# Kernel tuning notes

Hardware: AMD Instinct MI355X
Metric: run time of the kernel (lower is better)

## Reference

```python
import jax, jax.numpy as jnp
import numpy as np

N_NODES = 100000
N_EDGES = 600000
D_IN = 128
D_HID = 128
D_OUT = 64


def setup_inputs() -> dict:
    key = jax.random.key(0)
    ks = jax.random.split(key, 6)
    x = jax.random.normal(ks[0], (N_NODES, D_IN), dtype=jnp.float32)
    edge_index = jax.random.randint(ks[1], (2, N_EDGES), 0, N_NODES, dtype=jnp.int32)
    # Glorot-ish init for GCNConv weights
    W1 = jax.random.normal(ks[2], (D_IN, D_HID), dtype=jnp.float32) * (1.0 / np.sqrt(D_IN))
    W2 = jax.random.normal(ks[3], (D_HID, D_HID), dtype=jnp.float32) * (1.0 / np.sqrt(D_HID))
    W3 = jax.random.normal(ks[4], (D_HID, D_OUT), dtype=jnp.float32) * (1.0 / np.sqrt(D_HID))
    b1 = jnp.zeros((D_HID,), dtype=jnp.float32)
    b2 = jnp.zeros((D_HID,), dtype=jnp.float32)
    b3 = jnp.zeros((D_OUT,), dtype=jnp.float32)
    return {"x": x, "edge_index": edge_index, "W1": W1, "b1": b1,
            "W2": W2, "b2": b2, "W3": W3, "b3": b3}


def reference(x, edge_index, W1, b1, W2, b2, W3, b3):
    N = x.shape[0]
    # PyG GCNConv default: add self-loops, symmetric degree normalization.
    row, col = edge_index[0], edge_index[1]
    loops = jnp.arange(N, dtype=row.dtype)
    row = jnp.concatenate([row, loops])  # source nodes
    col = jnp.concatenate([col, loops])  # destination nodes (aggregation target)
    deg = jax.ops.segment_sum(jnp.ones(row.shape, dtype=x.dtype), col, num_segments=N)
    dinv = jax.lax.rsqrt(jnp.maximum(deg, 1.0))  # deg >= 1 due to self-loops
    norm = dinv[row] * dinv[col]  # [E+N]

    def gcn_conv(h, W, b):
        hw = h @ W                                   # dense transform [N, D]
        msg = hw[row] * norm[:, None]                # gather + normalize [E+N, D]
        return jax.ops.segment_sum(msg, col, num_segments=N) + b  # scatter-add

    h = jax.nn.relu(gcn_conv(x, W1, b1))
    # dropout p=0.5 is identity in eval mode (training=False)
    h = jax.nn.relu(gcn_conv(h, W2, b2))
    h = gcn_conv(h, W3, b3)
    return jax.nn.log_softmax(h, axis=1)
```

## Files before the change

### kernel.cpp

```cpp
#include <hip/hip_runtime.h>

#define NN 100000
#define NE 600000

typedef unsigned short u16;
typedef float f32x4 __attribute__((ext_vector_type(4)));
typedef short s16x8 __attribute__((ext_vector_type(8)));

__device__ inline u16 f2bf(float f) {
    unsigned u = __float_as_uint(f);
    return (u16)((u + 0x7FFFu + ((u >> 16) & 1u)) >> 16);
}
__device__ inline float bflo(unsigned u) { return __uint_as_float(u << 16); }
__device__ inline float bfhi(unsigned u) { return __uint_as_float(u & 0xFFFF0000u); }
__device__ inline unsigned pk(float a, float b) {
    return (unsigned)f2bf(a) | ((unsigned)f2bf(b) << 16);
}


__global__ void k_init_deg(int* __restrict__ deg, int n) {
    int i = blockIdx.x * 256 + threadIdx.x;
    if (i < n) deg[i] = 0;
}

__global__ void k_deg_count(const int* __restrict__ col, int* __restrict__ deg, int E) {
    int e = blockIdx.x * 256 + threadIdx.x;
    if (e < E) atomicAdd(&deg[col[e]], 1);
}

__global__ void k_scan1(const int* __restrict__ deg, int* __restrict__ offs,
                        int* __restrict__ bsums, float* __restrict__ dinv, int n) {
    __shared__ int s[256];
    int t = threadIdx.x;
    int i = blockIdx.x * 256 + t;
    int v = (i < n) ? deg[i] : 0;
    if (i < n) dinv[i] = rsqrtf((float)(v + 1));
    s[t] = v;
    __syncthreads();
    for (int off = 1; off < 256; off <<= 1) {
        int x = (t >= off) ? s[t - off] : 0;
        __syncthreads();
        s[t] += x;
        __syncthreads();
    }
    if (i < n) offs[i] = s[t] - v;
    if (t == 255) bsums[blockIdx.x] = s[255];
}

__global__ void k_scan2(int* __restrict__ bsums, int nb) {
    __shared__ int s[512];
    int t = threadIdx.x;
    int v = (t < nb) ? bsums[t] : 0;
    s[t] = v;
    __syncthreads();
    for (int off = 1; off < 512; off <<= 1) {
        int x = (t >= off) ? s[t - off] : 0;
        __syncthreads();
        s[t] += x;
        __syncthreads();
    }
    if (t < nb) bsums[t] = s[t] - v;
}

__global__ void k_scan3(int* __restrict__ offs, const int* __restrict__ bsums,
                        int* __restrict__ cursor, int n) {
    int i = blockIdx.x * 256 + threadIdx.x;
    if (i < n) {
        int o = offs[i] + bsums[i >> 8];
        offs[i] = o;
        cursor[i] = o;
    }
}

__global__ void k_fill(const int* __restrict__ row, const int* __restrict__ col,
                       int* __restrict__ cursor, int* __restrict__ srcs, int E) {
    int e = blockIdx.x * 256 + threadIdx.x;
    if (e < E) {
        int p = atomicAdd(&cursor[col[e]], 1);
        srcs[p] = row[e];
    }
}


__device__ inline void pack_one(const float* W, u16* Wp, int g, int DOUT) {
    int i  = g & 7;
    int l  = (g >> 3) & 63;
    int kk = (g >> 9) & 3;
    int t  = g >> 11;
    int k = kk * 32 + ((l >> 4) << 3) + i;
    int c = t * 16 + (l & 15);
    Wp[g] = f2bf(W[k * DOUT + c]);
}

__global__ __launch_bounds__(256)
void k_pack_all(const float* __restrict__ W1, const float* __restrict__ W2,
                const float* __restrict__ W3, u16* __restrict__ wp1,
                u16* __restrict__ wp2, u16* __restrict__ wp3) {
    int gid = blockIdx.x * 256 + threadIdx.x;
    if (gid < 16384) pack_one(W1, wp1, gid, 128);
    else if (gid < 32768) pack_one(W2, wp2, gid - 16384, 128);
    else if (gid < 40960) pack_one(W3, wp3, gid - 32768, 64);
}


template <int DOUT, bool OB16, bool AF32>
__global__ __launch_bounds__(256)
void k_gemm_mfma(const void* __restrict__ Hin, const u16* __restrict__ Wp,
                 const float* __restrict__ dinv, void* __restrict__ Gout, int n) {
    constexpr int NT = DOUT / 16;
    int tid = threadIdx.x;
    int w = tid >> 6, l = tid & 63;
    int r0 = blockIdx.x * 128 + w * 32;
    int arow0 = r0 + (l & 15);
    int arow1 = arow0 + 16;
    bool av0 = arow0 < n, av1 = arow1 < n;
    const s16x8* A0 = (const s16x8*)((const u16*)Hin + (size_t)arow0 * 128);
    const s16x8* A1 = (const s16x8*)((const u16*)Hin + (size_t)arow1 * 128);
    const float* A032 = (const float*)Hin + (size_t)arow0 * 128;
    const float* A132 = (const float*)Hin + (size_t)arow1 * 128;
    const s16x8* Wp8 = (const s16x8*)Wp;
    const s16x8 zero = {0, 0, 0, 0, 0, 0, 0, 0};

    f32x4 acc0[NT], acc1[NT];
#pragma unroll
    for (int t = 0; t < NT; t++) { acc0[t] = {0.f,0.f,0.f,0.f}; acc1[t] = {0.f,0.f,0.f,0.f}; }

#pragma unroll
    for (int kk = 0; kk < 4; kk++) {
        s16x8 a0, a1;
        if (AF32) {
            a0 = zero; a1 = zero;
            if (av0) {
                const f32x4* p = (const f32x4*)(A032 + kk * 32 + ((l >> 4) << 3));
                f32x4 f0 = p[0], f1 = p[1];
                a0[0]=(short)f2bf(f0[0]); a0[1]=(short)f2bf(f0[1]);
                a0[2]=(short)f2bf(f0[2]); a0[3]=(short)f2bf(f0[3]);
                a0[4]=(short)f2bf(f1[0]); a0[5]=(short)f2bf(f1[1]);
                a0[6]=(short)f2bf(f1[2]); a0[7]=(short)f2bf(f1[3]);
            }
            if (av1) {
                const f32x4* p = (const f32x4*)(A132 + kk * 32 + ((l >> 4) << 3));
                f32x4 f0 = p[0], f1 = p[1];
                a1[0]=(short)f2bf(f0[0]); a1[1]=(short)f2bf(f0[1]);
                a1[2]=(short)f2bf(f0[2]); a1[3]=(short)f2bf(f0[3]);
                a1[4]=(short)f2bf(f1[0]); a1[5]=(short)f2bf(f1[1]);
                a1[6]=(short)f2bf(f1[2]); a1[7]=(short)f2bf(f1[3]);
            }
        } else {
            a0 = av0 ? A0[kk * 4 + (l >> 4)] : zero;
            a1 = av1 ? A1[kk * 4 + (l >> 4)] : zero;
        }
#pragma unroll
        for (int t = 0; t < NT; t++) {
            s16x8 b = Wp8[(t * 4 + kk) * 64 + l];
            acc0[t] = __builtin_amdgcn_mfma_f32_16x16x32_bf16(a0, b, acc0[t], 0, 0, 0);
            acc1[t] = __builtin_amdgcn_mfma_f32_16x16x32_bf16(a1, b, acc1[t], 0, 0, 0);
        }
    }

    int col = l & 15;
#pragma unroll
    for (int r = 0; r < 4; r++) {
        int gr0 = r0 + (l >> 4) * 4 + r;
        if (gr0 < n) {
            float di = dinv[gr0];
#pragma unroll
            for (int t = 0; t < NT; t++) {
                float v = acc0[t][r] * di;
                if (OB16) ((u16*)Gout)[(size_t)gr0 * DOUT + t * 16 + col] = f2bf(v);
                else      ((float*)Gout)[(size_t)gr0 * DOUT + t * 16 + col] = v;
            }
        }
        int gr1 = gr0 + 16;
        if (gr1 < n) {
            float di = dinv[gr1];
#pragma unroll
            for (int t = 0; t < NT; t++) {
                float v = acc1[t][r] * di;
                if (OB16) ((u16*)Gout)[(size_t)gr1 * DOUT + t * 16 + col] = f2bf(v);
                else      ((float*)Gout)[(size_t)gr1 * DOUT + t * 16 + col] = v;
            }
        }
    }
}


#define ACC8(A, U) \
    A[0] += bflo(U.x); A[1] += bfhi(U.x); A[2] += bflo(U.y); A[3] += bfhi(U.y); \
    A[4] += bflo(U.z); A[5] += bfhi(U.z); A[6] += bflo(U.w); A[7] += bfhi(U.w);

__global__ __launch_bounds__(256)
void k_agg_relu(const uint4* __restrict__ G, const int* __restrict__ offs,
                const int* __restrict__ deg, const int* __restrict__ srcs,
                const float* __restrict__ dinv, const float* __restrict__ bias,
                uint4* __restrict__ out, int n) {
    int t = blockIdx.x * 256 + threadIdx.x;
    int wv = t >> 6;
    int lane = t & 63;
    int hl = lane & 15;
    int node = wv * 4 + (lane >> 4);
    if (node >= n) return;

    uint4 us = G[(size_t)node * 16 + hl];
    float a0[8], a1[8], a2[8], a3[8];
    a0[0] = bflo(us.x); a0[1] = bfhi(us.x); a0[2] = bflo(us.y); a0[3] = bfhi(us.y);
    a0[4] = bflo(us.z); a0[5] = bfhi(us.z); a0[6] = bflo(us.w); a0[7] = bfhi(us.w);
#pragma unroll
    for (int i = 0; i < 8; i++) { a1[i] = 0.f; a2[i] = 0.f; a3[i] = 0.f; }

    int start = offs[node];
    int cnt = deg[node];
    int j = 0;
    for (; j + 4 <= cnt; j += 4) {
        int s0 = srcs[start + j + 0];
        int s1 = srcs[start + j + 1];
        int s2 = srcs[start + j + 2];
        int s3 = srcs[start + j + 3];
        uint4 u0 = G[(size_t)s0 * 16 + hl];
        uint4 u1 = G[(size_t)s1 * 16 + hl];
        uint4 u2 = G[(size_t)s2 * 16 + hl];
        uint4 u3 = G[(size_t)s3 * 16 + hl];
        ACC8(a0, u0) ACC8(a1, u1) ACC8(a2, u2) ACC8(a3, u3)
    }
    for (; j < cnt; j++) {
        int s = srcs[start + j];
        uint4 u = G[(size_t)s * 16 + hl];
        ACC8(a0, u)
    }

    float di = dinv[node];
    const float4* b8 = (const float4*)bias;
    float4 b0 = b8[hl * 2], b1 = b8[hl * 2 + 1];
    float bb[8] = {b0.x, b0.y, b0.z, b0.w, b1.x, b1.y, b1.z, b1.w};
    float r[8];
#pragma unroll
    for (int i = 0; i < 8; i++) {
        float s = (a0[i] + a1[i]) + (a2[i] + a3[i]);
        r[i] = fmaxf(fmaf(s, di, bb[i]), 0.f);
    }
    out[(size_t)node * 16 + hl] =
        make_uint4(pk(r[0], r[1]), pk(r[2], r[3]), pk(r[4], r[5]), pk(r[6], r[7]));
}

#define ACC4(A, U) \
    A[0] += bflo(U.x); A[1] += bfhi(U.x); A[2] += bflo(U.y); A[3] += bfhi(U.y);

__global__ __launch_bounds__(256)
void k_agg_softmax(const uint2* __restrict__ G, const int* __restrict__ offs,
                   const int* __restrict__ deg, const int* __restrict__ srcs,
                   const float* __restrict__ dinv, const float* __restrict__ bias,
                   float4* __restrict__ out, int n) {
    int t = blockIdx.x * 256 + threadIdx.x;
    int wv = t >> 6;
    int lane = t & 63;
    int hl = lane & 15;
    int node = wv * 4 + (lane >> 4);
    if (node >= n) return;

    uint2 us = G[(size_t)node * 16 + hl];
    float a0[4], a1[4], a2[4], a3[4];
    a0[0] = bflo(us.x); a0[1] = bfhi(us.x); a0[2] = bflo(us.y); a0[3] = bfhi(us.y);
#pragma unroll
    for (int i = 0; i < 4; i++) { a1[i] = 0.f; a2[i] = 0.f; a3[i] = 0.f; }

    int start = offs[node];
    int cnt = deg[node];
    int j = 0;
    for (; j + 4 <= cnt; j += 4) {
        int s0 = srcs[start + j + 0];
        int s1 = srcs[start + j + 1];
        int s2 = srcs[start + j + 2];
        int s3 = srcs[start + j + 3];
        uint2 u0 = G[(size_t)s0 * 16 + hl];
        uint2 u1 = G[(size_t)s1 * 16 + hl];
        uint2 u2 = G[(size_t)s2 * 16 + hl];
        uint2 u3 = G[(size_t)s3 * 16 + hl];
        ACC4(a0, u0) ACC4(a1, u1) ACC4(a2, u2) ACC4(a3, u3)
    }
    for (; j < cnt; j++) {
        int s = srcs[start + j];
        uint2 u = G[(size_t)s * 16 + hl];
        ACC4(a0, u)
    }

    float di = dinv[node];
    float4 bb = ((const float4*)bias)[hl];
    float t0 = fmaf((a0[0] + a1[0]) + (a2[0] + a3[0]), di, bb.x);
    float t1 = fmaf((a0[1] + a1[1]) + (a2[1] + a3[1]), di, bb.y);
    float t2 = fmaf((a0[2] + a1[2]) + (a2[2] + a3[2]), di, bb.z);
    float t3 = fmaf((a0[3] + a1[3]) + (a2[3] + a3[3]), di, bb.w);
    float m = fmaxf(fmaxf(t0, t1), fmaxf(t2, t3));
#pragma unroll
    for (int off = 1; off < 16; off <<= 1) m = fmaxf(m, __shfl_xor(m, off, 64));
    float e = expf(t0 - m) + expf(t1 - m) + expf(t2 - m) + expf(t3 - m);
#pragma unroll
    for (int off = 1; off < 16; off <<= 1) e += __shfl_xor(e, off, 64);
    float lse = m + logf(e);
    out[(size_t)node * 16 + hl] = make_float4(t0 - lse, t1 - lse, t2 - lse, t3 - lse);
}


extern "C" void kernel_launch(void* const* d_in, const int* in_sizes, int n_in,
                              void* d_out, int out_size, void* d_ws, size_t ws_size,
                              hipStream_t stream) {
    const float* x  = (const float*)d_in[0];
    const int*   ei = (const int*)d_in[1];
    const int*   row = ei;
    const int*   col = ei + NE;
    const float* W1 = (const float*)d_in[2];
    const float* b1 = (const float*)d_in[3];
    const float* W2 = (const float*)d_in[4];
    const float* b2 = (const float*)d_in[5];
    const float* W3 = (const float*)d_in[6];
    const float* b3 = (const float*)d_in[7];
    float* outp = (float*)d_out;

    char* ws = (char*)d_ws;
    size_t off = 0;
    auto alloc = [&](size_t bytes) -> void* {
        void* p = (void*)(ws + off);
        off += (bytes + 255) & ~(size_t)255;
        return p;
    };
    float* dinv  = (float*)alloc((size_t)NN * 4);
    float* bufA  = (float*)alloc((size_t)NN * 128 * 4);
    u16*   bufB  = (u16*)alloc((size_t)NN * 128 * 2);
    int*   deg   = (int*)alloc((size_t)NN * 4);
    int*   offs  = (int*)alloc((size_t)NN * 4);
    int*   cursor= (int*)alloc((size_t)NN * 4);
    int*   bsums = (int*)alloc(1024 * 4);
    int*   srcs  = (int*)alloc((size_t)NE * 4);
    u16*   wp1   = (u16*)alloc(128 * 128 * 2);
    u16*   wp2   = (u16*)alloc(128 * 128 * 2);
    u16*   wp3   = (u16*)alloc(128 * 64 * 2);

    int nbN = (NN + 255) / 256;
    int nbE = (NE + 255) / 256;

    k_init_deg <<<nbN, 256, 0, stream>>>(deg, NN);
    k_deg_count<<<nbE, 256, 0, stream>>>(col, deg, NE);
    k_scan1    <<<nbN, 256, 0, stream>>>(deg, offs, bsums, dinv, NN);
    k_scan2    <<<1,   512, 0, stream>>>(bsums, nbN);
    k_scan3    <<<nbN, 256, 0, stream>>>(offs, bsums, cursor, NN);
    k_fill     <<<nbE, 256, 0, stream>>>(row, col, cursor, srcs, NE);
    k_pack_all <<<160, 256, 0, stream>>>(W1, W2, W3, wp1, wp2, wp3);

    int gb = (NN + 127) / 128;
    int ab4 = ((NN + 3) / 4 * 64 + 255) / 256;

    k_gemm_mfma<128, true, true><<<gb, 256, 0, stream>>>(x, wp1, dinv, bufA, NN);
    k_agg_relu <<<ab4, 256, 0, stream>>>((uint4*)bufA, offs, deg, srcs, dinv, b1, (uint4*)bufB, NN);
    k_gemm_mfma<128, true, false><<<gb, 256, 0, stream>>>(bufB, wp2, dinv, bufA, NN);
    k_agg_relu <<<ab4, 256, 0, stream>>>((uint4*)bufA, offs, deg, srcs, dinv, b2, (uint4*)bufB, NN);
    k_gemm_mfma<64, true, false><<<gb, 256, 0, stream>>>(bufB, wp3, dinv, bufA, NN);
    k_agg_softmax<<<ab4, 256, 0, stream>>>((uint2*)bufA, offs, deg, srcs, dinv, b3, (float4*)outp, NN);
}
```

Baseline: 310.8 us.

## Pad CSR neighbor lists to multiples of eight with zero sentinel row

Each node's CSR segment is rounded up to a multiple of eight and padded with a sentinel index pointing to a zeroed extra row of the feature buffer. The aggregation kernels can then load indices as two int4 vectors and issue eight gathers per iteration with no remainder loop. The layer-3 feature buffer now uses a row stride of 128 so the sentinel row lines up. This adds a padding kernel, larger index storage and wasted gathers on padded slots, and replaces the degree init kernel with a memset.

Measured after the change: 304.8 us. Within noise of the previous version (-1.9%).

```diff
diff --git a/kernel.cpp b/kernel.cpp
--- a/kernel.cpp
+++ b/kernel.cpp
@@ -17,11 +17,6 @@
     return (unsigned)f2bf(a) | ((unsigned)f2bf(b) << 16);
 }
 
-
-__global__ void k_init_deg(int* __restrict__ deg, int n) {
-    int i = blockIdx.x * 256 + threadIdx.x;
-    if (i < n) deg[i] = 0;
-}
 
 __global__ void k_deg_count(const int* __restrict__ col, int* __restrict__ deg, int E) {
     int e = blockIdx.x * 256 + threadIdx.x;
@@ -33,8 +28,9 @@
     __shared__ int s[256];
     int t = threadIdx.x;
     int i = blockIdx.x * 256 + t;
-    int v = (i < n) ? deg[i] : 0;
-    if (i < n) dinv[i] = rsqrtf((float)(v + 1));
+    int d = (i < n) ? deg[i] : 0;
+    int v = (i < n) ? (((d + 7) >> 3) << 3) : 0;
+    if (i < n) dinv[i] = rsqrtf((float)(d + 1));
     s[t] = v;
     __syncthreads();
     for (int off = 1; off < 256; off <<= 1) {
@@ -81,6 +77,17 @@
     }
 }
 
+__global__ void k_pad(const int* __restrict__ deg, const int* __restrict__ offs,
+                      int* __restrict__ srcs, int n) {
+    int i = blockIdx.x * 256 + threadIdx.x;
+    if (i < n) {
+        int d = deg[i];
+        int pd = ((d + 7) >> 3) << 3;
+        int o = offs[i] + d;
+        for (int j = d; j < pd; j++) srcs[o++] = NN;
+    }
+}
+
 
 __device__ inline void pack_one(const float* W, u16* Wp, int g, int DOUT) {
     int i  = g & 7;
@@ -95,11 +102,13 @@
 __global__ __launch_bounds__(256)
 void k_pack_all(const float* __restrict__ W1, const float* __restrict__ W2,
                 const float* __restrict__ W3, u16* __restrict__ wp1,
-                u16* __restrict__ wp2, u16* __restrict__ wp3) {
+                u16* __restrict__ wp2, u16* __restrict__ wp3,
+                uint4* __restrict__ bufA) {
     int gid = blockIdx.x * 256 + threadIdx.x;
     if (gid < 16384) pack_one(W1, wp1, gid, 128);
     else if (gid < 32768) pack_one(W2, wp2, gid - 16384, 128);
     else if (gid < 40960) pack_one(W3, wp3, gid - 32768, 64);
+    else if (gid < 40976) bufA[(size_t)NN * 16 + (gid - 40960)] = make_uint4(0, 0, 0, 0);
 }
 
 
@@ -167,8 +176,8 @@
 #pragma unroll
             for (int t = 0; t < NT; t++) {
                 float v = acc0[t][r] * di;
-                if (OB16) ((u16*)Gout)[(size_t)gr0 * DOUT + t * 16 + col] = f2bf(v);
-                else      ((float*)Gout)[(size_t)gr0 * DOUT + t * 16 + col] = v;
+                if (OB16) ((u16*)Gout)[(size_t)gr0 * 128 + t * 16 + col] = f2bf(v);
+                else      ((float*)Gout)[(size_t)gr0 * 128 + t * 16 + col] = v;
             }
         }
         int gr1 = gr0 + 16;
@@ -177,8 +186,8 @@
 #pragma unroll
             for (int t = 0; t < NT; t++) {
                 float v = acc1[t][r] * di;
-                if (OB16) ((u16*)Gout)[(size_t)gr1 * DOUT + t * 16 + col] = f2bf(v);
-                else      ((float*)Gout)[(size_t)gr1 * DOUT + t * 16 + col] = v;
+                if (OB16) ((u16*)Gout)[(size_t)gr1 * 128 + t * 16 + col] = f2bf(v);
+                else      ((float*)Gout)[(size_t)gr1 * 128 + t * 16 + col] = v;
             }
         }
     }
@@ -209,23 +218,20 @@
     for (int i = 0; i < 8; i++) { a1[i] = 0.f; a2[i] = 0.f; a3[i] = 0.f; }
 
     int start = offs[node];
-    int cnt = deg[node];
-    int j = 0;
-    for (; j + 4 <= cnt; j += 4) {
-        int s0 = srcs[start + j + 0];
-        int s1 = srcs[start + j + 1];
-        int s2 = srcs[start + j + 2];
-        int s3 = srcs[start + j + 3];
-        uint4 u0 = G[(size_t)s0 * 16 + hl];
-        uint4 u1 = G[(size_t)s1 * 16 + hl];
-        uint4 u2 = G[(size_t)s2 * 16 + hl];
-        uint4 u3 = G[(size_t)s3 * 16 + hl];
+    int nb = (deg[node] + 7) >> 3;
+    for (int b = 0; b < nb; b++) {
+        const int4* ip = (const int4*)&srcs[start + b * 8];
+        int4 i0 = ip[0], i1 = ip[1];
+        uint4 u0 = G[(size_t)i0.x * 16 + hl];
+        uint4 u1 = G[(size_t)i0.y * 16 + hl];
+        uint4 u2 = G[(size_t)i0.z * 16 + hl];
+        uint4 u3 = G[(size_t)i0.w * 16 + hl];
+        uint4 u4 = G[(size_t)i1.x * 16 + hl];
+        uint4 u5 = G[(size_t)i1.y * 16 + hl];
+        uint4 u6 = G[(size_t)i1.z * 16 + hl];
+        uint4 u7 = G[(size_t)i1.w * 16 + hl];
         ACC8(a0, u0) ACC8(a1, u1) ACC8(a2, u2) ACC8(a3, u3)
-    }
-    for (; j < cnt; j++) {
-        int s = srcs[start + j];
-        uint4 u = G[(size_t)s * 16 + hl];
-        ACC8(a0, u)
+        ACC8(a0, u4) ACC8(a1, u5) ACC8(a2, u6) ACC8(a3, u7)
     }
 
     float di = dinv[node];
@@ -257,30 +263,27 @@
     int node = wv * 4 + (lane >> 4);
     if (node >= n) return;
 
-    uint2 us = G[(size_t)node * 16 + hl];
+    uint2 us = G[(size_t)node * 32 + hl];
     float a0[4], a1[4], a2[4], a3[4];
     a0[0] = bflo(us.x); a0[1] = bfhi(us.x); a0[2] = bflo(us.y); a0[3] = bfhi(us.y);
 #pragma unroll
     for (int i = 0; i < 4; i++) { a1[i] = 0.f; a2[i] = 0.f; a3[i] = 0.f; }
 
     int start = offs[node];
-    int cnt = deg[node];
-    int j = 0;
-    for (; j + 4 <= cnt; j += 4) {
-        int s0 = srcs[start + j + 0];
-        int s1 = srcs[start + j + 1];
-        int s2 = srcs[start + j + 2];
-        int s3 = srcs[start + j + 3];
-        uint2 u0 = G[(size_t)s0 * 16 + hl];
-        uint2 u1 = G[(size_t)s1 * 16 + hl];
-        uint2 u2 = G[(size_t)s2 * 16 + hl];
-        uint2 u3 = G[(size_t)s3 * 16 + hl];
+    int nb = (deg[node] + 7) >> 3;
+    for (int b = 0; b < nb; b++) {
+        const int4* ip = (const int4*)&srcs[start + b * 8];
+        int4 i0 = ip[0], i1 = ip[1];
+        uint2 u0 = G[(size_t)i0.x * 32 + hl];
+        uint2 u1 = G[(size_t)i0.y * 32 + hl];
+        uint2 u2 = G[(size_t)i0.z * 32 + hl];
+        uint2 u3 = G[(size_t)i0.w * 32 + hl];
+        uint2 u4 = G[(size_t)i1.x * 32 + hl];
+        uint2 u5 = G[(size_t)i1.y * 32 + hl];
+        uint2 u6 = G[(size_t)i1.z * 32 + hl];
+        uint2 u7 = G[(size_t)i1.w * 32 + hl];
         ACC4(a0, u0) ACC4(a1, u1) ACC4(a2, u2) ACC4(a3, u3)
-    }
-    for (; j < cnt; j++) {
-        int s = srcs[start + j];
-        uint2 u = G[(size_t)s * 16 + hl];
-        ACC4(a0, u)
+        ACC4(a0, u4) ACC4(a1, u5) ACC4(a2, u6) ACC4(a3, u7)
     }
 
     float di = dinv[node];
@@ -329,7 +332,7 @@
     int*   offs  = (int*)alloc((size_t)NN * 4);
     int*   cursor= (int*)alloc((size_t)NN * 4);
     int*   bsums = (int*)alloc(1024 * 4);
-    int*   srcs  = (int*)alloc((size_t)NE * 4);
+    int*   srcs  = (int*)alloc(((size_t)NE + 7 * (size_t)NN + 8) * 4);
     u16*   wp1   = (u16*)alloc(128 * 128 * 2);
     u16*   wp2   = (u16*)alloc(128 * 128 * 2);
     u16*   wp3   = (u16*)alloc(128 * 64 * 2);
@@ -337,13 +340,14 @@
     int nbN = (NN + 255) / 256;
     int nbE = (NE + 255) / 256;
 
-    k_init_deg <<<nbN, 256, 0, stream>>>(deg, NN);
+    hipMemsetAsync(deg, 0, (size_t)NN * 4, stream);
     k_deg_count<<<nbE, 256, 0, stream>>>(col, deg, NE);
     k_scan1    <<<nbN, 256, 0, stream>>>(deg, offs, bsums, dinv, NN);
     k_scan2    <<<1,   512, 0, stream>>>(bsums, nbN);
     k_scan3    <<<nbN, 256, 0, stream>>>(offs, bsums, cursor, NN);
     k_fill     <<<nbE, 256, 0, stream>>>(row, col, cursor, srcs, NE);
-    k_pack_all <<<160, 256, 0, stream>>>(W1, W2, W3, wp1, wp2, wp3);
+    k_pad      <<<nbN, 256, 0, stream>>>(deg, offs, srcs, NN);
+    k_pack_all <<<161, 256, 0, stream>>>(W1, W2, W3, wp1, wp2, wp3, (uint4*)bufA);
 
     int gb = (NN + 127) / 128;
     int ab4 = ((NN + 3) / 4 * 64 + 255) / 256;
```
